# Kernel optimization log

Hardware: AMD Instinct MI355X
Metric: run time of the kernel (lower is better)

## Reference

```python
import jax, jax.numpy as jnp
import numpy as np

N_INPUTS = 1024
N_MIDDLE = 256
N_OUTPUTS = 64
BATCH = 65536


def setup_inputs() -> dict:
    key = jax.random.key(0)
    k_x, k_w1, k_w2 = jax.random.split(key, 3)
    x = jax.random.normal(k_x, (BATCH, N_INPUTS), dtype=jnp.float32)
    # Synapse weights k are initialized with random.random() in [0, 1)
    W1 = jax.random.uniform(k_w1, (N_MIDDLE, N_INPUTS), dtype=jnp.float32)
    W2 = jax.random.uniform(k_w2, (N_OUTPUTS, N_MIDDLE), dtype=jnp.float32)
    # Neuron biases b are initialized to 0.0
    b1 = jnp.zeros((N_MIDDLE,), dtype=jnp.float32)
    b2 = jnp.zeros((N_OUTPUTS,), dtype=jnp.float32)
    return {"x": x, "W1": W1, "b1": b1, "W2": W2, "b2": b2}


def reference(x, W1, b1, W2, b2):
    # Middle RegularNeurons: relu(sum_j k_ij * x_j + b_i)
    h = jax.nn.relu(jnp.einsum('bi,mi->bm', x, W1) + b1)  # [B, n_middle]
    # Output DestinationNeurons: relu(sum_m k_om * h_m + b_o)
    y = jax.nn.relu(jnp.einsum('bm,om->bo', h, W2) + b2)  # [B, n_outputs]
    return y
```

## Files before the change

kernel.cpp:

```cpp
#include <hip/hip_runtime.h>
#include <stdint.h>

#define NIN 1024
#define NMID 256
#define NOUT 64
#define BM 64
#define BK 32
#define NSTEP 32

typedef __attribute__((ext_vector_type(8))) short bf16x8;
typedef __attribute__((ext_vector_type(4))) float fx4;
typedef __attribute__((ext_vector_type(16))) float f32x16;
typedef __attribute__((ext_vector_type(4))) uint32_t u32x4;

#define XBUF 8192

union FragU { bf16x8 v; uint32_t u[4]; };

static __device__ __forceinline__ uint32_t cvtpk(float lo, float hi) {
  uint32_t r;
  asm("v_cvt_pk_bf16_f32 %0, %1, %2" : "=v"(r) : "v"(lo), "v"(hi));
  return r;
}
static __device__ __forceinline__ void gload16(const void* g, void* l) {
  __builtin_amdgcn_global_load_lds(
      (const __attribute__((address_space(1))) uint32_t*)g,
      (__attribute__((address_space(3))) uint32_t*)l, 16, 0, 0);
}

#define VMCNT2() asm volatile("s_waitcnt vmcnt(2)" ::: "memory")
#define SBAR()   __builtin_amdgcn_s_barrier()
#define SFENCE() __builtin_amdgcn_sched_barrier(0)

__global__ __launch_bounds__(256) void cvt_weights(
    const float* __restrict__ W1, const float* __restrict__ W2,
    unsigned short* __restrict__ w1f, unsigned short* __restrict__ w2b) {
  int gid = blockIdx.x * 256 + threadIdx.x;
  if (gid < 32768) {
    int r = gid & 31;
    int kb = (gid >> 5) & 127;
    int c = gid >> 12;
    const float* s = W1 + (size_t)(c * 32 + r) * NIN + kb * 8;
    fx4 v0 = *(const fx4*)s;
    fx4 v1 = *(const fx4*)(s + 4);
    u32x4 o = {cvtpk(v0.x, v0.y), cvtpk(v0.z, v0.w),
               cvtpk(v1.x, v1.y), cvtpk(v1.z, v1.w)};
    *(u32x4*)(w1f + (size_t)gid * 8) = o;
  } else {
    int e2 = (gid - 32768) << 2;
    if (e2 < NOUT * NMID) {
      fx4 v = *(const fx4*)(W2 + e2);
      uint2 p; p.x = cvtpk(v.x, v.y); p.y = cvtpk(v.z, v.w);
      *(uint2*)(w2b + e2) = p;
    }
  }
}

__global__ __launch_bounds__(256, 4) void livenet_main(
    const float* __restrict__ x,
    const unsigned short* __restrict__ w1f,
    const float* __restrict__ b1,
    const unsigned short* __restrict__ w2b,
    const float* __restrict__ b2,
    float* __restrict__ y) {

  __shared__ __align__(16) char smem[32768];

  const int tid = threadIdx.x;
  const int lane = tid & 63;
  const int w = tid >> 6;
  const int wn = w;
  const int l31 = lane & 31;
  const int lh = lane >> 5;
  const int row0 = blockIdx.x * BM;

  uint32_t xsrc[2], xdst[2];
#pragma unroll
  for (int i = 0; i < 2; ++i) {
    uint32_t o = (uint32_t)(i * 4096 + tid * 16);
    uint32_t r = o >> 7;
    uint32_t pcn = (o >> 4) & 7u;
    uint32_t j = pcn ^ (r & 7u);
    xsrc[i] = (uint32_t)(row0 + (int)r) * NIN + j * 4u;
    xdst[i] = o;
  }

#define XSTAGE(b3, k0)                                          \
  { char* xb_ = smem + (b3) * XBUF;                             \
    gload16(x + xsrc[0] + (k0), xb_ + xdst[0]);                 \
    gload16(x + xsrc[1] + (k0), xb_ + xdst[1]); }

  f32x16 acc[2][2];
#pragma unroll
  for (int mt = 0; mt < 2; ++mt)
#pragma unroll
    for (int nt = 0; nt < 2; ++nt)
#pragma unroll
      for (int q = 0; q < 16; ++q) acc[mt][nt][q] = 0.f;

  const char* wbase0 = (const char*)(w1f + ((size_t)(wn * 2 + 0) * 4096 + l31) * 8) + lh * 512;
  const char* wbase1 = (const char*)(w1f + ((size_t)(wn * 2 + 1) * 4096 + l31) * 8) + lh * 512;

  const uint32_t arx = (uint32_t)(l31 & 7);
  const uint32_t ar0 = (uint32_t)(l31) * 128u;
  const uint32_t ar1 = (uint32_t)(32 + l31) * 128u;

  XSTAGE(0, 0);
  XSTAGE(1, BK);

  int b3 = 0;
  for (int t = 0; t < NSTEP; ++t) {
    VMCNT2();
    SBAR();
    SFENCE();

    const char* xb = smem + b3 * XBUF;
    const int tb = t * 2048;

    bf16x8 bfr[2][2];
#pragma unroll
    for (int kf = 0; kf < 2; ++kf) {
      bfr[0][kf] = *(const bf16x8*)(wbase0 + tb + kf * 1024);
      bfr[1][kf] = *(const bf16x8*)(wbase1 + tb + kf * 1024);
    }

    if (t < NSTEP - 2) {
      int nb = b3 + 2; if (nb >= 3) nb -= 3;
      XSTAGE(nb, (t + 2) * BK);
    }

#pragma unroll
    for (int kf = 0; kf < 2; ++kf) {
      uint32_t j0 = (uint32_t)(kf * 4 + lh * 2);
      fx4 va = *(const fx4*)(xb + ar0 + ((j0 ^ arx) << 4));
      fx4 vb = *(const fx4*)(xb + ar0 + (((j0 + 1) ^ arx) << 4));
      fx4 vc = *(const fx4*)(xb + ar1 + ((j0 ^ arx) << 4));
      fx4 vd = *(const fx4*)(xb + ar1 + (((j0 + 1) ^ arx) << 4));
      FragU f, g;
      f.u[0] = cvtpk(va.x, va.y); f.u[1] = cvtpk(va.z, va.w);
      f.u[2] = cvtpk(vb.x, vb.y); f.u[3] = cvtpk(vb.z, vb.w);
      g.u[0] = cvtpk(vc.x, vc.y); g.u[1] = cvtpk(vc.z, vc.w);
      g.u[2] = cvtpk(vd.x, vd.y); g.u[3] = cvtpk(vd.z, vd.w);
      __builtin_amdgcn_s_setprio(1);
      acc[0][0] = __builtin_amdgcn_mfma_f32_32x32x16_bf16(f.v, bfr[0][kf], acc[0][0], 0, 0, 0);
      acc[0][1] = __builtin_amdgcn_mfma_f32_32x32x16_bf16(f.v, bfr[1][kf], acc[0][1], 0, 0, 0);
      acc[1][0] = __builtin_amdgcn_mfma_f32_32x32x16_bf16(g.v, bfr[0][kf], acc[1][0], 0, 0, 0);
      acc[1][1] = __builtin_amdgcn_mfma_f32_32x32x16_bf16(g.v, bfr[1][kf], acc[1][1], 0, 0, 0);
      __builtin_amdgcn_s_setprio(0);
    }

    ++b3; if (b3 >= 3) b3 -= 3;
  }
  __syncthreads();

  float b1v[2];
#pragma unroll
  for (int nt = 0; nt < 2; ++nt) b1v[nt] = b1[wn * 64 + nt * 32 + l31];

#pragma unroll
  for (int mt = 0; mt < 2; ++mt) {
#pragma unroll
    for (int nt = 0; nt < 2; ++nt) {
      int col = wn * 64 + nt * 32 + l31;
#pragma unroll
      for (int rg = 0; rg < 16; ++rg) {
        int row = mt * 32 + (rg & 3) + 8 * (rg >> 2) + 4 * lh;
        float v = acc[mt][nt][rg] + b1v[nt];
        v = v > 0.f ? v : 0.f;
        int j = (col >> 3) ^ (row & 31);
        *(unsigned short*)(smem + row * 512 + (j << 4) + (col & 7) * 2) =
            (unsigned short)cvtpk(v, v);
      }
    }
  }
  __syncthreads();

  f32x16 acc2;
#pragma unroll
  for (int q = 0; q < 16; ++q) acc2[q] = 0.f;

  const int r2 = (w >> 1) * 32;
  const int c2 = (w & 1) * 32;
  const int arow = r2 + l31;
  const uint32_t arx2 = (uint32_t)(arow & 31);
  const unsigned short* w2row = w2b + (size_t)(c2 + l31) * NMID + lh * 8;

#pragma unroll
  for (int kk = 0; kk < 16; ++kk) {
    bf16x8 a2 = *(const bf16x8*)(smem + arow * 512 +
                                 ((((uint32_t)(kk * 2 + lh)) ^ arx2) << 4));
    bf16x8 bw = *(const bf16x8*)(w2row + kk * 16);
    acc2 = __builtin_amdgcn_mfma_f32_32x32x16_bf16(a2, bw, acc2, 0, 0, 0);
  }

  float bias2 = b2[c2 + l31];
#pragma unroll
  for (int rg = 0; rg < 16; ++rg) {
    int row = r2 + (rg & 3) + 8 * (rg >> 2) + 4 * lh;
    float v = acc2[rg] + bias2;
    v = v > 0.f ? v : 0.f;
    y[(size_t)(row0 + row) * NOUT + c2 + l31] = v;
  }
}

extern "C" void kernel_launch(void* const* d_in, const int* in_sizes, int n_in,
                              void* d_out, int out_size, void* d_ws, size_t ws_size,
                              hipStream_t stream) {
  const float* x  = (const float*)d_in[0];
  const float* W1 = (const float*)d_in[1];
  const float* b1 = (const float*)d_in[2];
  const float* W2 = (const float*)d_in[3];
  const float* b2 = (const float*)d_in[4];
  float* y = (float*)d_out;

  unsigned short* w1f = (unsigned short*)d_ws;
  unsigned short* w2b = w1f + (size_t)NMID * NIN;

  const int batch = in_sizes[0] / NIN;

  hipLaunchKernelGGL(cvt_weights, dim3(144), dim3(256), 0, stream,
                     W1, W2, w1f, w2b);
  hipLaunchKernelGGL(livenet_main, dim3(batch / BM), dim3(256), 0, stream,
                     x, w1f, b1, w2b, b2, y);
}
```

Before: 79.61 us.

## Prefetch W1 fragments two steps ahead in double-buffered registers

The bf16 W1 fragments are now loaded into two alternating register sets (bP/bQ), two k-steps ahead of the MFMAs that use them, instead of being loaded at the top of each iteration. The main loop is unrolled by six so the LDS ring-buffer indices and register sets are compile-time constants. The vmcnt wait is raised to 6 so it counts both the in-flight x stages and the weight loads, with a full drain on the last step. This hides global-load latency for the weights, at the cost of 16 extra VGPRs per thread and a larger unrolled body that may pressure occupancy at launch bounds 4.

```diff
diff --git a/kernel.cpp b/kernel.cpp
--- a/kernel.cpp
+++ b/kernel.cpp
@@ -28,7 +28,6 @@
       (__attribute__((address_space(3))) uint32_t*)l, 16, 0, 0);
 }
 
-#define VMCNT2() asm volatile("s_waitcnt vmcnt(2)" ::: "memory")
 #define SBAR()   __builtin_amdgcn_s_barrier()
 #define SFENCE() __builtin_amdgcn_sched_barrier(0)
 
@@ -105,52 +104,58 @@
   const uint32_t ar0 = (uint32_t)(l31) * 128u;
   const uint32_t ar1 = (uint32_t)(32 + l31) * 128u;
 
+  bf16x8 bP[4], bQ[4];
+
+#define BLOAD(SET, T)                                           \
+  { const char* w0_ = wbase0 + (size_t)(T) * 2048;              \
+    const char* w1_ = wbase1 + (size_t)(T) * 2048;              \
+    SET[0] = *(const bf16x8*)(w0_);                             \
+    SET[1] = *(const bf16x8*)(w0_ + 1024);                      \
+    SET[2] = *(const bf16x8*)(w1_);                             \
+    SET[3] = *(const bf16x8*)(w1_ + 1024); }
+
+#define ITER(T, CBUF, NBUF, SET, WAITN)                                     \
+  { asm volatile("s_waitcnt vmcnt(" #WAITN ")" ::: "memory");               \
+    SBAR();                                                                 \
+    SFENCE();                                                               \
+    if ((T) < NSTEP - 2) { XSTAGE(NBUF, ((T) + 2) * BK); }                  \
+    const char* xb_ = smem + (CBUF) * XBUF;                                 \
+    _Pragma("unroll") for (int kf = 0; kf < 2; ++kf) {                      \
+      uint32_t j0 = (uint32_t)(kf * 4 + lh * 2);                            \
+      fx4 va = *(const fx4*)(xb_ + ar0 + ((j0 ^ arx) << 4));                \
+      fx4 vb = *(const fx4*)(xb_ + ar0 + (((j0 + 1) ^ arx) << 4));          \
+      fx4 vc = *(const fx4*)(xb_ + ar1 + ((j0 ^ arx) << 4));                \
+      fx4 vd = *(const fx4*)(xb_ + ar1 + (((j0 + 1) ^ arx) << 4));          \
+      FragU f, g;                                                           \
+      f.u[0] = cvtpk(va.x, va.y); f.u[1] = cvtpk(va.z, va.w);               \
+      f.u[2] = cvtpk(vb.x, vb.y); f.u[3] = cvtpk(vb.z, vb.w);               \
+      g.u[0] = cvtpk(vc.x, vc.y); g.u[1] = cvtpk(vc.z, vc.w);               \
+      g.u[2] = cvtpk(vd.x, vd.y); g.u[3] = cvtpk(vd.z, vd.w);               \
+      __builtin_amdgcn_s_setprio(1);                                        \
+      acc[0][0] = __builtin_amdgcn_mfma_f32_32x32x16_bf16(f.v, SET[kf],     acc[0][0], 0, 0, 0); \
+      acc[0][1] = __builtin_amdgcn_mfma_f32_32x32x16_bf16(f.v, SET[2 + kf], acc[0][1], 0, 0, 0); \
+      acc[1][0] = __builtin_amdgcn_mfma_f32_32x32x16_bf16(g.v, SET[kf],     acc[1][0], 0, 0, 0); \
+      acc[1][1] = __builtin_amdgcn_mfma_f32_32x32x16_bf16(g.v, SET[2 + kf], acc[1][1], 0, 0, 0); \
+      __builtin_amdgcn_s_setprio(0);                                        \
+    }                                                                       \
+    if ((T) < NSTEP - 2) { BLOAD(SET, (T) + 2); } }
+
   XSTAGE(0, 0);
+  BLOAD(bP, 0);
   XSTAGE(1, BK);
-
-  int b3 = 0;
-  for (int t = 0; t < NSTEP; ++t) {
-    VMCNT2();
-    SBAR();
-    SFENCE();
-
-    const char* xb = smem + b3 * XBUF;
-    const int tb = t * 2048;
-
-    bf16x8 bfr[2][2];
-#pragma unroll
-    for (int kf = 0; kf < 2; ++kf) {
-      bfr[0][kf] = *(const bf16x8*)(wbase0 + tb + kf * 1024);
-      bfr[1][kf] = *(const bf16x8*)(wbase1 + tb + kf * 1024);
-    }
-
-    if (t < NSTEP - 2) {
-      int nb = b3 + 2; if (nb >= 3) nb -= 3;
-      XSTAGE(nb, (t + 2) * BK);
-    }
-
-#pragma unroll
-    for (int kf = 0; kf < 2; ++kf) {
-      uint32_t j0 = (uint32_t)(kf * 4 + lh * 2);
-      fx4 va = *(const fx4*)(xb + ar0 + ((j0 ^ arx) << 4));
-      fx4 vb = *(const fx4*)(xb + ar0 + (((j0 + 1) ^ arx) << 4));
-      fx4 vc = *(const fx4*)(xb + ar1 + ((j0 ^ arx) << 4));
-      fx4 vd = *(const fx4*)(xb + ar1 + (((j0 + 1) ^ arx) << 4));
-      FragU f, g;
-      f.u[0] = cvtpk(va.x, va.y); f.u[1] = cvtpk(va.z, va.w);
-      f.u[2] = cvtpk(vb.x, vb.y); f.u[3] = cvtpk(vb.z, vb.w);
-      g.u[0] = cvtpk(vc.x, vc.y); g.u[1] = cvtpk(vc.z, vc.w);
-      g.u[2] = cvtpk(vd.x, vd.y); g.u[3] = cvtpk(vd.z, vd.w);
-      __builtin_amdgcn_s_setprio(1);
-      acc[0][0] = __builtin_amdgcn_mfma_f32_32x32x16_bf16(f.v, bfr[0][kf], acc[0][0], 0, 0, 0);
-      acc[0][1] = __builtin_amdgcn_mfma_f32_32x32x16_bf16(f.v, bfr[1][kf], acc[0][1], 0, 0, 0);
-      acc[1][0] = __builtin_amdgcn_mfma_f32_32x32x16_bf16(g.v, bfr[0][kf], acc[1][0], 0, 0, 0);
-      acc[1][1] = __builtin_amdgcn_mfma_f32_32x32x16_bf16(g.v, bfr[1][kf], acc[1][1], 0, 0, 0);
-      __builtin_amdgcn_s_setprio(0);
-    }
-
-    ++b3; if (b3 >= 3) b3 -= 3;
-  }
+  BLOAD(bQ, 1);
+
+  for (int t0 = 0; t0 < 30; t0 += 6) {
+    ITER(t0 + 0, 0, 2, bP, 6);
+    ITER(t0 + 1, 1, 0, bQ, 6);
+    ITER(t0 + 2, 2, 1, bP, 6);
+    ITER(t0 + 3, 0, 2, bQ, 6);
+    ITER(t0 + 4, 1, 0, bP, 6);
+    ITER(t0 + 5, 2, 1, bQ, 6);
+  }
+  ITER(30, 0, 2, bP, 6);
+  ITER(31, 1, 0, bQ, 0);
+
   __syncthreads();
 
   float b1v[2];
```

Measured after the change: 84.65 us. 6.3% more time.
